# Performance work log

Measured on AMD Instinct MI355X. Metric: run time of the kernel, lower is better.

Reference implementation:

```python
import jax, jax.numpy as jnp
import numpy as np

N = 200000
E = 600000
C = 256


def setup_inputs() -> dict:
    key = jax.random.key(0)
    k1, k2, k3, k4, k5 = jax.random.split(key, 5)
    x = jax.random.normal(k1, (N, C), dtype=jnp.float32)
    sources = jax.random.randint(k2, (E,), 0, N, dtype=jnp.int64)
    targets = jax.random.randint(k3, (E,), 0, N, dtype=jnp.int64)
    norm = jax.random.uniform(k4, (N, 1), dtype=jnp.float32)
    # xavier_normal for [C, C]: std = sqrt(2 / (fan_in + fan_out))
    std = float(np.sqrt(2.0 / (C + C)))
    weight = jax.random.normal(k5, (C, C), dtype=jnp.float32) * std
    return {"x": x, "sources": sources, "targets": targets, "norm": norm, "weight": weight}


def reference(x, sources, targets, norm, weight):
    # out-of-place index_add: x + scatter_add(x[sources] -> targets)
    agg = x.at[targets].add(x[sources])  # [N, C]
    h = norm * agg                        # [N, C], norm broadcasts over channels
    return h @ weight                     # [N, C]
```

## Files before the change

### kernel.cpp

```cpp
#include <hip/hip_runtime.h>
#include <hip/hip_bf16.h>

#define NN 200000
#define NE 600000
#define CH 256
#define NBLK_SCAN 196
#define ZW_TILES 6250

typedef short bf16x8 __attribute__((ext_vector_type(8)));
typedef float f32x4 __attribute__((ext_vector_type(4)));
typedef unsigned short ushort8v __attribute__((ext_vector_type(8)));

__device__ __forceinline__ unsigned short f2bf(float f) {
    unsigned int u = __builtin_bit_cast(unsigned int, f);
    u = (u + 0x7FFFu + ((u >> 16) & 1u)) >> 16;
    return (unsigned short)u;
}
__device__ __forceinline__ float bf2f(unsigned short u) {
    unsigned int v = ((unsigned int)u) << 16;
    return __builtin_bit_cast(float, v);
}

__global__ void k_wt(const float* __restrict__ W, unsigned short* __restrict__ Wt) {
    int j = blockIdx.x, k = threadIdx.x;
    Wt[j * CH + k] = f2bf(W[k * CH + j]);
}

__global__ __launch_bounds__(256) void k_prep(const float* __restrict__ W,
                                              unsigned short* __restrict__ Wt,
                                              const int* __restrict__ te,
                                              int* __restrict__ deg) {
    const int t = blockIdx.x * 256 + threadIdx.x;
    const int S = gridDim.x * 256;
    for (int e = t; e < NE; e += S) atomicAdd(&deg[te[e]], 1);
    for (int i = t; i < CH * CH; i += S) {
        int j = i >> 8, k = i & 255;
        Wt[j * CH + k] = f2bf(W[k * CH + j]);
    }
}

__global__ __launch_bounds__(256) void k_scanA(const int* __restrict__ deg,
                                               int* __restrict__ off,
                                               int* __restrict__ bsum) {
    __shared__ int ts[256];
    int tid = threadIdx.x;
    int base = blockIdx.x * 1024 + tid * 4;
    int v[4];
#pragma unroll
    for (int j = 0; j < 4; ++j) {
        int idx = base + j;
        v[j] = (idx < NN) ? deg[idx] : 0;
    }
    int tsum = v[0] + v[1] + v[2] + v[3];
    ts[tid] = tsum;
    __syncthreads();
    int x = tsum;
    for (int ofs = 1; ofs < 256; ofs <<= 1) {
        int y = (tid >= ofs) ? ts[tid - ofs] : 0;
        __syncthreads();
        x += y;
        ts[tid] = x;
        __syncthreads();
    }
    int run = x - tsum;
#pragma unroll
    for (int j = 0; j < 4; ++j) {
        int idx = base + j;
        if (idx < NN) off[idx] = run;
        run += v[j];
    }
    if (tid == 255) bsum[blockIdx.x] = x;
}

__global__ __launch_bounds__(256) void k_scanC(int* __restrict__ off,
                                               const int* __restrict__ bsum,
                                               int* __restrict__ cur) {
    __shared__ int ts[256];
    int tid = threadIdx.x;
    int v = (tid < NBLK_SCAN) ? bsum[tid] : 0;
    ts[tid] = v;
    __syncthreads();
    int x = v;
    for (int ofs = 1; ofs < 256; ofs <<= 1) {
        int y = (tid >= ofs) ? ts[tid - ofs] : 0;
        __syncthreads();
        x += y;
        ts[tid] = x;
        __syncthreads();
    }
    const int bo = (blockIdx.x == 0) ? 0 : ts[blockIdx.x - 1];
    int base = blockIdx.x * 1024 + tid * 4;
#pragma unroll
    for (int j = 0; j < 4; ++j) {
        int idx = base + j;
        if (idx < NN) {
            int o = off[idx] + bo;
            off[idx] = o;
            cur[idx] = o;
        }
    }
}

__global__ void k_fill(const int* __restrict__ se, const int* __restrict__ te,
                       int* __restrict__ cur, int* __restrict__ elist) {
    int e = blockIdx.x * 256 + threadIdx.x;
    if (e < NE) {
        int t = te[e];
        int pos = atomicAdd(&cur[t], 1);
        elist[pos] = se[e];
    }
}

__global__ __launch_bounds__(256, 4) void k_zw(const float* __restrict__ x,
                                               const unsigned short* __restrict__ Wt,
                                               unsigned short* __restrict__ zbf,
                                               const int* __restrict__ te,
                                               int* __restrict__ deg) {
    __shared__ unsigned short lds_a[32 * CH];
    const int tid = threadIdx.x;
    const int wid = tid >> 6;
    const int lane = tid & 63;
    const int r16 = lane & 15;
    const int q = lane >> 4;
    const int rb = blockIdx.x * 32;

    {
        const int e = blockIdx.x * 256 + tid;
        if (e < NE) atomicAdd(&deg[te[e]], 1);
    }

    const float* gx = x + (size_t)rb * CH;
    float4 st0[4], st1[4];
#pragma unroll
    for (int i = 0; i < 4; ++i) {
        const int idx = i * 2048 + tid * 8;
        st0[i] = *reinterpret_cast<const float4*>(gx + idx);
        st1[i] = *reinterpret_cast<const float4*>(gx + idx + 4);
    }
#pragma unroll
    for (int i = 0; i < 4; ++i) {
        const int idx = i * 2048 + tid * 8;
        const int row = idx >> 8;
        const int col = idx & 255;
        ushort8v w;
        w[0] = f2bf(st0[i].x); w[1] = f2bf(st0[i].y);
        w[2] = f2bf(st0[i].z); w[3] = f2bf(st0[i].w);
        w[4] = f2bf(st1[i].x); w[5] = f2bf(st1[i].y);
        w[6] = f2bf(st1[i].z); w[7] = f2bf(st1[i].w);
        const int gs = (col >> 3) ^ (row & 7);
        *reinterpret_cast<ushort8v*>(&lds_a[row * CH + gs * 8]) = w;
    }
    __syncthreads();

    f32x4 acc[2][4];
#pragma unroll
    for (int m = 0; m < 2; ++m)
#pragma unroll
        for (int nt = 0; nt < 4; ++nt) acc[m][nt] = (f32x4){0.f, 0.f, 0.f, 0.f};

    const unsigned short* wb = Wt + (size_t)(wid * 64 + r16) * CH + q * 8;

#pragma unroll
    for (int kk = 0; kk < 8; ++kk) {
        bf16x8 b[4];
#pragma unroll
        for (int nt = 0; nt < 4; ++nt)
            b[nt] = *reinterpret_cast<const bf16x8*>(wb + (size_t)nt * 16 * CH + kk * 32);
        bf16x8 a[2];
#pragma unroll
        for (int m = 0; m < 2; ++m) {
            const int lr = m * 16 + r16;
            const int aidx = lr * CH + ((((kk * 4) + q) ^ (lr & 7)) << 3);
            a[m] = *reinterpret_cast<const bf16x8*>(&lds_a[aidx]);
        }
#pragma unroll
        for (int m = 0; m < 2; ++m)
#pragma unroll
            for (int nt = 0; nt < 4; ++nt)
                acc[m][nt] = __builtin_amdgcn_mfma_f32_16x16x32_bf16(a[m], b[nt], acc[m][nt], 0, 0, 0);
    }

#pragma unroll
    for (int m = 0; m < 2; ++m) {
#pragma unroll
        for (int nt = 0; nt < 4; ++nt) {
            unsigned short* po = zbf + (size_t)(rb + m * 16 + q * 4) * CH
                               + wid * 64 + nt * 16 + r16;
#pragma unroll
            for (int r = 0; r < 4; ++r) po[(size_t)r * CH] = f2bf(acc[m][nt][r]);
        }
    }
}

__global__ __launch_bounds__(256) void k_gout(const unsigned short* __restrict__ zbf,
                                              const int* __restrict__ off,
                                              const int* __restrict__ deg,
                                              const int* __restrict__ elist,
                                              const float* __restrict__ norm,
                                              float* __restrict__ out) {
    int wid = threadIdx.x >> 6;
    int lane = threadIdx.x & 63;
    int row = blockIdx.x * 4 + wid;
    if (row >= NN) return;
    int start = off[row];
    int d = deg[row];
    const int uo = lane * 4;
    ushort4 bv = *reinterpret_cast<const ushort4*>(zbf + (size_t)row * CH + uo);
    float ax = bf2f(bv.x), ay = bf2f(bv.y), az = bf2f(bv.z), aw = bf2f(bv.w);
    int e = 0;
    while (e < d) {
        int i0 = (e + 0 < d) ? elist[start + e + 0] : -1;
        int i1 = (e + 1 < d) ? elist[start + e + 1] : -1;
        int i2 = (e + 2 < d) ? elist[start + e + 2] : -1;
        int i3 = (e + 3 < d) ? elist[start + e + 3] : -1;
        int i4 = (e + 4 < d) ? elist[start + e + 4] : -1;
        int i5 = (e + 5 < d) ? elist[start + e + 5] : -1;
        int i6 = (e + 6 < d) ? elist[start + e + 6] : -1;
        int i7 = (e + 7 < d) ? elist[start + e + 7] : -1;
#define GACC(ii) if (ii >= 0) { \
            ushort4 v = *reinterpret_cast<const ushort4*>(zbf + (size_t)ii * CH + uo); \
            ax += bf2f(v.x); ay += bf2f(v.y); az += bf2f(v.z); aw += bf2f(v.w); }
        GACC(i0) GACC(i1) GACC(i2) GACC(i3) GACC(i4) GACC(i5) GACC(i6) GACC(i7)
#undef GACC
        e += 8;
    }
    const float nv = norm[row];
    float4 o;
    o.x = ax * nv; o.y = ay * nv; o.z = az * nv; o.w = aw * nv;
    *reinterpret_cast<float4*>(out + (size_t)row * CH + uo) = o;
}

__global__ __launch_bounds__(256, 4) void k_fgg(const float* __restrict__ x,
                                                const int* __restrict__ off,
                                                const int* __restrict__ deg,
                                                const int* __restrict__ elist,
                                                const float* __restrict__ norm,
                                                const unsigned short* __restrict__ Wt,
                                                float* __restrict__ out) {
    __shared__ unsigned short lds_a[64 * CH];
    const int tid = threadIdx.x;
    const int wid = tid >> 6;
    const int lane = tid & 63;
    const int rb = blockIdx.x * 64;
    const int rowbase = rb + wid * 16;
    const int r16 = lane & 15;
    const int q = lane >> 4;
    const int fo4 = lane * 4;

    const int offv = off[rowbase + r16];
    const int degv = deg[rowbase + r16];
    const float nv = norm[rb + lane];

    float4 acc[16];
#pragma unroll
    for (int r = 0; r < 16; ++r)
        acc[r] = *reinterpret_cast<const float4*>(x + (size_t)(rowbase + r) * CH + fo4);

#pragma unroll
    for (int r = 0; r < 16; ++r) {
        const int start = __shfl(offv, r);
        const int d = __shfl(degv, r);
        int e = 0;
        while (e < d) {
            int i0 = (e + 0 < d) ? elist[start + e + 0] : -1;
            int i1 = (e + 1 < d) ? elist[start + e + 1] : -1;
            int i2 = (e + 2 < d) ? elist[start + e + 2] : -1;
            int i3 = (e + 3 < d) ? elist[start + e + 3] : -1;
#define GACC(ii) if (ii >= 0) { \
            float4 v = *reinterpret_cast<const float4*>(x + (size_t)ii * CH + fo4); \
            acc[r].x += v.x; acc[r].y += v.y; acc[r].z += v.z; acc[r].w += v.w; }
            GACC(i0) GACC(i1) GACC(i2) GACC(i3)
#undef GACC
            e += 4;
        }
    }

    unsigned short* lb = lds_a + wid * 16 * CH;
#pragma unroll
    for (int r = 0; r < 16; ++r) {
        ushort4 w;
        w.x = f2bf(acc[r].x); w.y = f2bf(acc[r].y);
        w.z = f2bf(acc[r].z); w.w = f2bf(acc[r].w);
        const int gs = (lane >> 1) ^ (r & 7);
        *reinterpret_cast<ushort4*>(lb + r * CH + gs * 8 + (lane & 1) * 4) = w;
    }
    __syncthreads();

    f32x4 facc[4][4];
#pragma unroll
    for (int m = 0; m < 4; ++m)
#pragma unroll
        for (int nt = 0; nt < 4; ++nt) facc[m][nt] = (f32x4){0.f, 0.f, 0.f, 0.f};

    const unsigned short* wb = Wt + (size_t)(wid * 64 + r16) * CH + q * 8;

#pragma unroll
    for (int kk = 0; kk < 8; ++kk) {
        bf16x8 b[4];
#pragma unroll
        for (int nt = 0; nt < 4; ++nt)
            b[nt] = *reinterpret_cast<const bf16x8*>(wb + (size_t)nt * 16 * CH + kk * 32);
        bf16x8 a[4];
#pragma unroll
        for (int m = 0; m < 4; ++m) {
            const int lr = m * 16 + r16;
            const int idx = lr * CH + ((((kk * 4) + q) ^ (lr & 7)) << 3);
            a[m] = *reinterpret_cast<const bf16x8*>(&lds_a[idx]);
        }
#pragma unroll
        for (int m = 0; m < 4; ++m)
#pragma unroll
            for (int nt = 0; nt < 4; ++nt)
                facc[m][nt] = __builtin_amdgcn_mfma_f32_16x16x32_bf16(a[m], b[nt], facc[m][nt], 0, 0, 0);
    }

#pragma unroll
    for (int m = 0; m < 4; ++m) {
        const int crow = rb + m * 16 + q * 4;
#pragma unroll
        for (int nt = 0; nt < 4; ++nt) {
            float* po = out + (size_t)crow * CH + wid * 64 + nt * 16 + r16;
#pragma unroll
            for (int r = 0; r < 4; ++r) {
                const float nj = __shfl(nv, m * 16 + q * 4 + r);
                po[(size_t)r * CH] = facc[m][nt][r] * nj;
            }
        }
    }
}

extern "C" void kernel_launch(void* const* d_in, const int* in_sizes, int n_in,
                              void* d_out, int out_size, void* d_ws, size_t ws_size,
                              hipStream_t stream) {
    const float* x = (const float*)d_in[0];
    const int* se = (const int*)d_in[1];
    const int* te = (const int*)d_in[2];
    const float* norm = (const float*)d_in[3];
    const float* W = (const float*)d_in[4];
    float* out = (float*)d_out;

    char* ws = (char*)d_ws;
    unsigned short* Wt = (unsigned short*)ws;
    int* deg   = (int*)(ws + 131072);
    int* off   = (int*)(ws + 931072);
    int* cur   = (int*)(ws + 1731072);
    int* elist = (int*)(ws + 2531072);
    int* bsum  = (int*)(ws + 4931072);
    const size_t ZBF_OFF = 4932096;
    const size_t NEED = ZBF_OFF + (size_t)NN * CH * 2;
    const bool big = (ws_size >= NEED);
    unsigned short* zbf = (unsigned short*)(ws + ZBF_OFF);

    hipMemsetAsync(deg, 0, NN * sizeof(int), stream);
    if (big) {
        k_wt<<<CH, CH, 0, stream>>>(W, Wt);
        k_zw<<<ZW_TILES, 256, 0, stream>>>(x, Wt, zbf, te, deg);
        k_scanA<<<NBLK_SCAN, 256, 0, stream>>>(deg, off, bsum);
        k_scanC<<<NBLK_SCAN, 256, 0, stream>>>(off, bsum, cur);
        k_fill<<<(NE + 255) / 256, 256, 0, stream>>>(se, te, cur, elist);
        k_gout<<<NN / 4, 256, 0, stream>>>(zbf, off, deg, elist, norm, out);
    } else {
        k_prep<<<512, 256, 0, stream>>>(W, Wt, te, deg);
        k_scanA<<<NBLK_SCAN, 256, 0, stream>>>(deg, off, bsum);
        k_scanC<<<NBLK_SCAN, 256, 0, stream>>>(off, bsum, cur);
        k_fill<<<(NE + 255) / 256, 256, 0, stream>>>(se, te, cur, elist);
        k_fgg<<<NN / 64, 256, 0, stream>>>(x, off, deg, elist, norm, Wt, out);
    }
}
```

Baseline: 293.0 us.

## Restructure x@W tile kernel to load A straight into registers without LDS

The dense x·W kernel is reorganised so that each wave computes 16 full rows across all 256 output columns. The wave loads its fp32 slice of x directly into registers and converts it to bf16 for the MFMA operands, so the LDS staging buffer and its barrier go away. Blocks now cover 64 rows, and the occupancy hint drops from 4 to 3 to make room for the larger register footprint. In exchange, every wave re-reads the whole transposed weight matrix from cache, which raises L2 traffic and register pressure.

```diff
diff --git a/kernel.cpp b/kernel.cpp
--- a/kernel.cpp
+++ b/kernel.cpp
@@ -5,7 +5,6 @@
 #define NE 600000
 #define CH 256
 #define NBLK_SCAN 196
-#define ZW_TILES 6250
 
 typedef short bf16x8 __attribute__((ext_vector_type(8)));
 typedef float f32x4 __attribute__((ext_vector_type(4)));
@@ -111,84 +110,61 @@
     }
 }
 
-__global__ __launch_bounds__(256, 4) void k_zw(const float* __restrict__ x,
+__global__ __launch_bounds__(256, 3) void k_zw(const float* __restrict__ x,
                                                const unsigned short* __restrict__ Wt,
                                                unsigned short* __restrict__ zbf,
                                                const int* __restrict__ te,
                                                int* __restrict__ deg) {
-    __shared__ unsigned short lds_a[32 * CH];
     const int tid = threadIdx.x;
     const int wid = tid >> 6;
     const int lane = tid & 63;
     const int r16 = lane & 15;
     const int q = lane >> 4;
-    const int rb = blockIdx.x * 32;
 
     {
         const int e = blockIdx.x * 256 + tid;
         if (e < NE) atomicAdd(&deg[te[e]], 1);
     }
 
-    const float* gx = x + (size_t)rb * CH;
-    float4 st0[4], st1[4];
-#pragma unroll
-    for (int i = 0; i < 4; ++i) {
-        const int idx = i * 2048 + tid * 8;
-        st0[i] = *reinterpret_cast<const float4*>(gx + idx);
-        st1[i] = *reinterpret_cast<const float4*>(gx + idx + 4);
-    }
-#pragma unroll
-    for (int i = 0; i < 4; ++i) {
-        const int idx = i * 2048 + tid * 8;
-        const int row = idx >> 8;
-        const int col = idx & 255;
-        ushort8v w;
-        w[0] = f2bf(st0[i].x); w[1] = f2bf(st0[i].y);
-        w[2] = f2bf(st0[i].z); w[3] = f2bf(st0[i].w);
-        w[4] = f2bf(st1[i].x); w[5] = f2bf(st1[i].y);
-        w[6] = f2bf(st1[i].z); w[7] = f2bf(st1[i].w);
-        const int gs = (col >> 3) ^ (row & 7);
-        *reinterpret_cast<ushort8v*>(&lds_a[row * CH + gs * 8]) = w;
-    }
-    __syncthreads();
-
-    f32x4 acc[2][4];
-#pragma unroll
-    for (int m = 0; m < 2; ++m)
-#pragma unroll
-        for (int nt = 0; nt < 4; ++nt) acc[m][nt] = (f32x4){0.f, 0.f, 0.f, 0.f};
-
-    const unsigned short* wb = Wt + (size_t)(wid * 64 + r16) * CH + q * 8;
-
+    const int rb = blockIdx.x * 64 + wid * 16;
+    const float* arow = x + (size_t)(rb + r16) * CH + q * 8;
+
+    float4 pf[16];
 #pragma unroll
     for (int kk = 0; kk < 8; ++kk) {
-        bf16x8 b[4];
-#pragma unroll
-        for (int nt = 0; nt < 4; ++nt)
-            b[nt] = *reinterpret_cast<const bf16x8*>(wb + (size_t)nt * 16 * CH + kk * 32);
-        bf16x8 a[2];
-#pragma unroll
-        for (int m = 0; m < 2; ++m) {
-            const int lr = m * 16 + r16;
-            const int aidx = lr * CH + ((((kk * 4) + q) ^ (lr & 7)) << 3);
-            a[m] = *reinterpret_cast<const bf16x8*>(&lds_a[aidx]);
-        }
-#pragma unroll
-        for (int m = 0; m < 2; ++m)
-#pragma unroll
-            for (int nt = 0; nt < 4; ++nt)
-                acc[m][nt] = __builtin_amdgcn_mfma_f32_16x16x32_bf16(a[m], b[nt], acc[m][nt], 0, 0, 0);
-    }
-
-#pragma unroll
-    for (int m = 0; m < 2; ++m) {
-#pragma unroll
-        for (int nt = 0; nt < 4; ++nt) {
-            unsigned short* po = zbf + (size_t)(rb + m * 16 + q * 4) * CH
-                               + wid * 64 + nt * 16 + r16;
-#pragma unroll
-            for (int r = 0; r < 4; ++r) po[(size_t)r * CH] = f2bf(acc[m][nt][r]);
-        }
+        pf[2 * kk]     = *reinterpret_cast<const float4*>(arow + kk * 32);
+        pf[2 * kk + 1] = *reinterpret_cast<const float4*>(arow + kk * 32 + 4);
+    }
+#pragma unroll
+    for (int i = 0; i < 16; ++i)
+        asm volatile("" : "+v"(pf[i].x), "+v"(pf[i].y), "+v"(pf[i].z), "+v"(pf[i].w));
+
+    f32x4 acc[16];
+#pragma unroll
+    for (int nt = 0; nt < 16; ++nt) acc[nt] = (f32x4){0.f, 0.f, 0.f, 0.f};
+
+    const unsigned short* wb = Wt + (size_t)r16 * CH + q * 8;
+
+#pragma unroll
+    for (int kk = 0; kk < 8; ++kk) {
+        bf16x8 af;
+        af[0] = (short)f2bf(pf[2 * kk].x);     af[1] = (short)f2bf(pf[2 * kk].y);
+        af[2] = (short)f2bf(pf[2 * kk].z);     af[3] = (short)f2bf(pf[2 * kk].w);
+        af[4] = (short)f2bf(pf[2 * kk + 1].x); af[5] = (short)f2bf(pf[2 * kk + 1].y);
+        af[6] = (short)f2bf(pf[2 * kk + 1].z); af[7] = (short)f2bf(pf[2 * kk + 1].w);
+#pragma unroll
+        for (int nt = 0; nt < 16; ++nt) {
+            bf16x8 b = *reinterpret_cast<const bf16x8*>(wb + (size_t)nt * 16 * CH + kk * 32);
+            acc[nt] = __builtin_amdgcn_mfma_f32_16x16x32_bf16(af, b, acc[nt], 0, 0, 0);
+        }
+    }
+
+    const int crow = rb + q * 4;
+#pragma unroll
+    for (int nt = 0; nt < 16; ++nt) {
+        unsigned short* po = zbf + (size_t)crow * CH + nt * 16 + r16;
+#pragma unroll
+        for (int r = 0; r < 4; ++r) po[(size_t)r * CH] = f2bf(acc[nt][r]);
     }
 }
 
@@ -354,7 +330,7 @@
     hipMemsetAsync(deg, 0, NN * sizeof(int), stream);
     if (big) {
         k_wt<<<CH, CH, 0, stream>>>(W, Wt);
-        k_zw<<<ZW_TILES, 256, 0, stream>>>(x, Wt, zbf, te, deg);
+        k_zw<<<NN / 64, 256, 0, stream>>>(x, Wt, zbf, te, deg);
         k_scanA<<<NBLK_SCAN, 256, 0, stream>>>(deg, off, bsum);
         k_scanC<<<NBLK_SCAN, 256, 0, stream>>>(off, bsum, cur);
         k_fill<<<(NE + 255) / 256, 256, 0, stream>>>(se, te, cur, elist);
```

New measurement: 414.9 us. +41.6%, slower.
